# Optimization experiments

Measured on AMD Instinct MI355X. Metric: run time of the kernel, lower is better.

Reference implementation:

```python
import jax, jax.numpy as jnp
import numpy as np

TOP_K = 8
THRESHOLD = 0.0        # similarity_threshold
SELF_SIM = 0.999       # exclude_self cutoff
EPS = 1e-12            # F.normalize eps


def _l2_normalize(x):
    # matches torch.nn.functional.normalize(p=2, dim=-1, eps=1e-12)
    n = jnp.linalg.norm(x, axis=-1, keepdims=True)
    return x / jnp.maximum(n, EPS)


def setup_inputs() -> dict:
    key = jax.random.key(0)
    kq, km = jax.random.split(key)
    B, N, D = 2048, 65536, 512
    q = jax.random.normal(kq, (B, D), dtype=jnp.float32)
    mem = jax.random.normal(km, (N, D), dtype=jnp.float32)
    # add_memories() stores L2-normalized representations when normalize=True
    mem = _l2_normalize(mem)
    return {"query_representations": q, "memory_bank": mem}


def reference(query_representations, memory_bank):
    # normalize queries (config.normalize_memories=True)
    q = _l2_normalize(query_representations)            # [B, D]
    # cosine similarity: bank rows already unit-norm
    sims = jnp.einsum("bd,nd->bn", q, memory_bank)      # [B, N]
    neg_inf = jnp.float32(-jnp.inf)
    # exclude_self: mask near-exact matches
    sims = jnp.where(sims > SELF_SIM, neg_inf, sims)
    # threshold mask
    sims = jnp.where(sims >= THRESHOLD, sims, neg_inf)
    # top-k (k = min(top_k, count) = TOP_K since bank is full)
    top_sims, top_idx = jax.lax.top_k(sims, TOP_K)      # [B, K]
    retrieved = memory_bank[top_idx]                    # [B, K, D] gather
    mask = top_sims > neg_inf                           # [B, K] valid entries
    return retrieved, top_sims, mask
```

## Files before the change

kernel.cpp:

```cpp
#include <hip/hip_runtime.h>
#include <math.h>

#define D        512
#define NQ       2048
#define NMEM     65536
#define TOPK     8
#define NCAND    32
#define SELF_SIM 0.999f
#define FSCALE   64.0f
#define TAU_RAW  483.328f
#define CAP      448
#define SCAP     768

#define QB     128
#define SPAN   1024
#define NROUND 32
#define BUFSZ  16384u

typedef __attribute__((ext_vector_type(4))) float f32x4;
typedef __attribute__((ext_vector_type(4))) int   i32x4;
typedef __attribute__((ext_vector_type(8))) int   i32x8;

__device__ __forceinline__ void gl_lds16(const void* g, void* l) {
    __builtin_amdgcn_global_load_lds(
        (const __attribute__((address_space(1))) void*)g,
        (__attribute__((address_space(3))) void*)l, 16, 0, 0);
}

__device__ __forceinline__ unsigned pack4_fp8(float4 v) {
    int lo = __builtin_amdgcn_cvt_pk_fp8_f32(v.x * FSCALE, v.y * FSCALE, 0, false);
    return (unsigned)__builtin_amdgcn_cvt_pk_fp8_f32(v.z * FSCALE, v.w * FSCALE, lo, true);
}

__global__ __launch_bounds__(256)
void k_prep(const float* __restrict__ mem, const float* __restrict__ q,
            unsigned* __restrict__ mp8, unsigned* __restrict__ qp8,
            double* __restrict__ qinv)
{
    if (blockIdx.x < 2048) {
        const int i = blockIdx.x * 256 + threadIdx.x;
        const int row = i >> 3, p = i & 7;
        const float4* pf = (const float4*)(mem + (size_t)row * D + p * 64);
        float4 f[16];
        #pragma unroll
        for (int t = 0; t < 16; ++t) f[t] = pf[t];
        const int nblk = row >> 7, t8 = (row >> 4) & 7, fc = row & 15;
        const int kq = p >> 1, fb = (p & 1) * 2;
        uint4* dst = (uint4*)mp8 + ((size_t)nblk * 4096 + kq * 1024 + t8 * 128);
        #pragma unroll
        for (int u = 0; u < 2; ++u)
            #pragma unroll
            for (int h = 0; h < 2; ++h) {
                uint4 c;
                c.x = pack4_fp8(f[u * 8 + h * 4 + 0]);
                c.y = pack4_fp8(f[u * 8 + h * 4 + 1]);
                c.z = pack4_fp8(f[u * 8 + h * 4 + 2]);
                c.w = pack4_fp8(f[u * 8 + h * 4 + 3]);
                dst[h * 64 + (fb + u) * 16 + fc] = c;
            }
    } else {
        __shared__ float rb[4][512];
        const int wv = threadIdx.x >> 6, lane = threadIdx.x & 63;
        const int row = (blockIdx.x - 2048) * 4 + wv;
        const float4* src = (const float4*)(q + (size_t)row * D);
        float4 v0 = src[lane];
        float4 v1 = src[lane + 64];
        double ss = (double)v0.x*v0.x + (double)v0.y*v0.y + (double)v0.z*v0.z + (double)v0.w*v0.w
                  + (double)v1.x*v1.x + (double)v1.y*v1.y + (double)v1.z*v1.z + (double)v1.w*v1.w;
        #pragma unroll
        for (int off = 32; off >= 1; off >>= 1)
            ss += __shfl_xor(ss, off, 64);
        double inv = 1.0 / fmax(sqrt(ss), 1e-12);
        float invf = (float)inv;
        ((float4*)rb[wv])[lane]      = make_float4(v0.x*invf, v0.y*invf, v0.z*invf, v0.w*invf);
        ((float4*)rb[wv])[lane + 64] = make_float4(v1.x*invf, v1.y*invf, v1.z*invf, v1.w*invf);
        if (lane == 0) qinv[row] = inv;
        __syncthreads();
        if (lane < 32) {
            const int kq = lane >> 3, fr = (lane >> 1) & 3, h = lane & 1;
            const float* f = rb[wv] + kq * 128 + fr * 32 + h * 16;
            uint4 c;
            c.x = pack4_fp8(*(const float4*)(f));
            c.y = pack4_fp8(*(const float4*)(f + 4));
            c.z = pack4_fp8(*(const float4*)(f + 8));
            c.w = pack4_fp8(*(const float4*)(f + 12));
            const int qblk = row >> 6, t4 = (row >> 4) & 3, fc = row & 15;
            ((uint4*)qp8)[(size_t)qblk * 2048 + kq * 512 + t4 * 128 + h * 64 + fr * 16 + fc] = c;
        }
    }
}

__global__ __launch_bounds__(256, 4)
void k_cand(const char* __restrict__ qp8, const char* __restrict__ mp8,
            unsigned* __restrict__ cnt, uint2* __restrict__ cbuf)
{
    __shared__ __align__(16) char smem[32768 + 16 + SCAP * 8];
    unsigned* scnt = (unsigned*)(smem + 32768);
    uint2*    sbuf = (uint2*)   (smem + 32784);

    const int tid = threadIdx.x;
    const int w = tid >> 6, l = tid & 63;
    const int fc = l & 15, fr = l >> 4;

    const int id  = blockIdx.x;
    const int xcd = id & 7;
    const int j   = id >> 3;
    const int qblk = j & 15;
    const int sg   = j >> 4;
    const int split = xcd + 8 * sg;
    const int qbase = qblk * QB;
    const int nbase = split * SPAN;

    const char* qpan = qp8 + (size_t)(qblk * 2 + (w >> 1)) * 32768u
                           + (unsigned)(w & 1) * 4096u + (unsigned)l * 16u;
    const unsigned mpanel = (unsigned)(nbase >> 7) * 65536u;

    if (tid == 0) *scnt = 0u;

    f32x4 acc[2][8];
    const int lofs = l * 16;

#define STAGE(R, B)                                                            \
    {   const unsigned r_ = (unsigned)(R);                                     \
        const unsigned base_ = mpanel + (r_ >> 2) * 65536u + (r_ & 3u) * 16384u; \
        gl_lds16(mp8 + base_ + (unsigned)tid * 16u,          smem + (B) + (unsigned)tid * 16u); \
        gl_lds16(mp8 + base_ + (unsigned)tid * 16u + 4096u,  smem + (B) + (unsigned)tid * 16u + 4096u); \
        gl_lds16(mp8 + base_ + (unsigned)tid * 16u + 8192u,  smem + (B) + (unsigned)tid * 16u + 8192u); \
        gl_lds16(mp8 + base_ + (unsigned)tid * 16u + 12288u, smem + (B) + (unsigned)tid * 16u + 12288u); \
    }

    unsigned cb = 0u;
    STAGE(0, cb);

    for (int r = 0; r < NROUND; ++r) {
        const int kq = r & 3, sub = r >> 2;
        if (kq == 0) {
            #pragma unroll
            for (int jj = 0; jj < 2; ++jj)
                #pragma unroll
                for (int t = 0; t < 8; ++t) acc[jj][t] = (f32x4){0.f, 0.f, 0.f, 0.f};
        }
        asm volatile("" ::: "memory");
        __builtin_amdgcn_s_barrier();
        asm volatile("" ::: "memory");
        i32x4 qa0, qa1, qb0, qb1;
        {
            const char* qa = qpan + (unsigned)kq * 8192u;
            asm volatile("global_load_dwordx4 %0, %1, off"             : "=v"(qa0) : "v"(qa) : "memory");
            asm volatile("global_load_dwordx4 %0, %1, off offset:1024" : "=v"(qa1) : "v"(qa) : "memory");
            asm volatile("global_load_dwordx4 %0, %1, off offset:2048" : "=v"(qb0) : "v"(qa) : "memory");
            asm volatile("global_load_dwordx4 %0, %1, off offset:3072" : "=v"(qb1) : "v"(qa) : "memory");
        }
        if (r + 1 < NROUND) {
            STAGE(r + 1, cb ^ BUFSZ);
            asm volatile("s_waitcnt vmcnt(4)" ::: "memory");
        } else {
            asm volatile("s_waitcnt vmcnt(0)" ::: "memory");
        }
        __builtin_amdgcn_sched_barrier(0);
        __builtin_amdgcn_s_barrier();
        asm volatile("" ::: "memory");

        {
            const char* Ms = smem + cb;
            const i32x8 bv0 = __builtin_shufflevector(qa0, qa1, 0, 1, 2, 3, 4, 5, 6, 7);
            const i32x8 bv1 = __builtin_shufflevector(qb0, qb1, 0, 1, 2, 3, 4, 5, 6, 7);
            __builtin_amdgcn_s_setprio(1);
            #pragma unroll
            for (int t = 0; t < 8; ++t) {
                i32x4 lo = *(const i32x4*)(Ms + t * 2048 + lofs);
                i32x4 hi = *(const i32x4*)(Ms + t * 2048 + 1024 + lofs);
                i32x8 av = __builtin_shufflevector(lo, hi, 0, 1, 2, 3, 4, 5, 6, 7);
                acc[0][t] = __builtin_amdgcn_mfma_scale_f32_16x16x128_f8f6f4(
                              av, bv0, acc[0][t], 0, 0, 0, 0x7F7F7F7F, 0, 0x7F7F7F7F);
                acc[1][t] = __builtin_amdgcn_mfma_scale_f32_16x16x128_f8f6f4(
                              av, bv1, acc[1][t], 0, 0, 0, 0x7F7F7F7F, 0, 0x7F7F7F7F);
            }
            __builtin_amdgcn_s_setprio(0);
        }
        if (kq == 3) {
            const int nb0 = nbase + sub * 128 + fr * 4;
            #pragma unroll
            for (int jj = 0; jj < 2; ++jj) {
                const unsigned qloc = (unsigned)(w * 32 + jj * 16 + fc);
                #pragma unroll
                for (int t = 0; t < 8; ++t) {
                    const float tm = fmaxf(fmaxf(acc[jj][t][0], acc[jj][t][1]),
                                           fmaxf(acc[jj][t][2], acc[jj][t][3]));
                    if (tm > TAU_RAW) {
                        #pragma unroll
                        for (int rr = 0; rr < 4; ++rr) {
                            const float v = acc[jj][t][rr];
                            if (v > TAU_RAW) {
                                unsigned p = atomicAdd(scnt, 1u);
                                if (p < SCAP)
                                    sbuf[p] = make_uint2(__float_as_uint(v),
                                        (qloc << 16) | (unsigned)(nb0 + t * 16 + rr));
                            }
                        }
                    }
                }
            }
        }
        cb ^= BUFSZ;
    }
#undef STAGE

    __syncthreads();
    const unsigned ns = min(*scnt, (unsigned)SCAP);
    for (unsigned i = tid; i < ns; i += 256) {
        const uint2 e = sbuf[i];
        const int qg = qbase + (int)(e.y >> 16);
        const unsigned p = atomicAdd(&cnt[qg], 1u);
        if (p < CAP)
            cbuf[(size_t)qg * CAP + p] = make_uint2(e.x, e.y & 0xffffu);
    }
}

__global__ __launch_bounds__(256)
void k_final(const unsigned* __restrict__ cnt, const uint2* __restrict__ cbuf,
             const float* __restrict__ q, const float* __restrict__ mem,
             const double* __restrict__ qinv, float* __restrict__ out)
{
    __shared__ unsigned long long keys[CAP];
    __shared__ int    scand[NCAND];
    __shared__ double rsv[NCAND];
    __shared__ int    fidx[TOPK];

    const int qq  = blockIdx.x;
    const int tid = threadIdx.x;
    const int n = (int)min(cnt[qq], (unsigned)CAP);

    if (tid < NCAND) scand[tid] = -1;
    const uint2* src = cbuf + (size_t)qq * CAP;
    for (int c = tid; c < n; c += 256) {
        const uint2 e = src[c];
        keys[c] = ((unsigned long long)e.x << 16)
                | (unsigned long long)(0xffffu - (e.y & 0xffffu));
    }
    __syncthreads();
    for (int c = tid; c < n; c += 256) {
        const unsigned long long my = keys[c];
        int rank = 0;
        for (int j2 = 0; j2 < n; ++j2) rank += (keys[j2] > my) ? 1 : 0;
        if (rank < NCAND) scand[rank] = 0xffff - (int)(my & 0xffffu);
    }
    __syncthreads();

    const int w = tid >> 6, lane = tid & 63;
    float qv[8];
    #pragma unroll
    for (int t = 0; t < 8; ++t) qv[t] = q[(size_t)qq * D + t * 64 + lane];
    for (int ci = w * 8; ci < w * 8 + 8; ++ci) {
        const int m = scand[ci];
        double s = 0.0;
        if (m >= 0) {
            const float* mp = mem + (size_t)m * D;
            #pragma unroll
            for (int t = 0; t < 8; ++t)
                s += (double)qv[t] * (double)mp[t * 64 + lane];
        }
        #pragma unroll
        for (int off = 32; off >= 1; off >>= 1)
            s += __shfl_xor(s, off, 64);
        if (lane == 0) rsv[ci] = (m >= 0) ? s * qinv[qq] : -1.0 / 0.0;
    }
    __syncthreads();

    if (tid < NCAND) {
        double x = rsv[tid];
        if (scand[tid] < 0 || x > (double)SELF_SIM || x < 0.0) x = -1.0 / 0.0;
        rsv[tid] = x;
    }
    __syncthreads();
    if (tid < NCAND) {
        const double x  = rsv[tid];
        const int    mi = (scand[tid] < 0) ? 0x7fffffff : scand[tid];
        int rank = 0;
        for (int j2 = 0; j2 < NCAND; ++j2) {
            const double xj = rsv[j2];
            const int    ij = (scand[j2] < 0) ? 0x7fffffff : scand[j2];
            if (xj > x || (xj == x && (ij < mi || (ij == mi && j2 < tid)))) ++rank;
        }
        if (rank < TOPK) {
            float* tops  = out + (size_t)NQ * TOPK * D;
            float* maskp = tops + (size_t)NQ * TOPK;
            tops [qq * TOPK + rank] = (float)x;
            maskp[qq * TOPK + rank] = (x == -INFINITY) ? 0.0f : 1.0f;
            fidx [rank] = (scand[tid] < 0) ? 0 : scand[tid];
        }
    }
    __syncthreads();

    for (int i = tid; i < TOPK * (D / 4); i += 256) {
        const int s2 = i >> 7;
        const int d4 = i & 127;
        const int sr = fidx[s2];
        ((float4*)out)[((size_t)qq * TOPK + s2) * (D / 4) + d4] =
            ((const float4*)mem)[(size_t)sr * (D / 4) + d4];
    }
}

extern "C" void kernel_launch(void* const* d_in, const int* in_sizes, int n_in,
                              void* d_out, int out_size, void* d_ws, size_t ws_size,
                              hipStream_t stream)
{
    const float* q   = (const float*)d_in[0];
    const float* mem = (const float*)d_in[1];
    float* out = (float*)d_out;
    char* ws = (char*)d_ws;

    unsigned* mp8  = (unsigned*)(ws);
    unsigned* qp8  = (unsigned*)(ws + ((size_t)32 << 20));
    unsigned* cnt  = (unsigned*)(ws + ((size_t)33 << 20));
    uint2*    cbuf = (uint2*)   (ws + ((size_t)34 << 20));
    double*   qinv = (double*)  (ws + ((size_t)42 << 20));

    hipMemsetAsync(cnt, 0, NQ * sizeof(unsigned), stream);

    k_prep<<<2560, 256, 0, stream>>>(mem, q, mp8, qp8, qinv);
    k_cand<<<(NQ / QB) * (NMEM / SPAN), 256, 0, stream>>>((const char*)qp8, (const char*)mp8, cnt, cbuf);
    k_final<<<NQ, 256, 0, stream>>>(cnt, cbuf, q, mem, qinv, out);
}
```

Baseline: 185.0 us.

## Stage query tiles in LDS and split candidate kernel across 8 waves

The candidate kernel now runs 512 threads per block. Query fp8 panels are staged into LDS alongside memory panels through global_load_lds, replacing the per-wave direct global loads. The 8 waves split the block's 128 queries and 128 memory rows into 4x2 groups, so each wave holds half the accumulators. The per-query counter memset is folded into the prep kernel, which removes one launch. The trade-off is double the LDS footprint, which can lower occupancy, and larger barrier groups.

```diff
diff --git a/kernel.cpp b/kernel.cpp
--- a/kernel.cpp
+++ b/kernel.cpp
@@ -15,7 +15,7 @@
 #define QB     128
 #define SPAN   1024
 #define NROUND 32
-#define BUFSZ  16384u
+#define BUFSZ  32768u
 
 typedef __attribute__((ext_vector_type(4))) float f32x4;
 typedef __attribute__((ext_vector_type(4))) int   i32x4;
@@ -32,12 +32,21 @@
     return (unsigned)__builtin_amdgcn_cvt_pk_fp8_f32(v.z * FSCALE, v.w * FSCALE, lo, true);
 }
 
+__device__ __forceinline__ i32x8 ldpair(const char* p) {
+    const i32x4 a = *(const i32x4*)p;
+    const i32x4 b = *(const i32x4*)(p + 1024);
+    return __builtin_shufflevector(a, b, 0, 1, 2, 3, 4, 5, 6, 7);
+}
+
 __global__ __launch_bounds__(256)
 void k_prep(const float* __restrict__ mem, const float* __restrict__ q,
             unsigned* __restrict__ mp8, unsigned* __restrict__ qp8,
-            double* __restrict__ qinv)
+            double* __restrict__ qinv, unsigned* __restrict__ cnt)
 {
     if (blockIdx.x < 2048) {
+        if (blockIdx.x == 0) {
+            for (int c = threadIdx.x; c < NQ; c += 256) cnt[c] = 0u;
+        }
         const int i = blockIdx.x * 256 + threadIdx.x;
         const int row = i >> 3, p = i & 7;
         const float4* pf = (const float4*)(mem + (size_t)row * D + p * 64);
@@ -90,17 +99,18 @@
     }
 }
 
-__global__ __launch_bounds__(256, 4)
+__global__ __launch_bounds__(512, 4)
 void k_cand(const char* __restrict__ qp8, const char* __restrict__ mp8,
             unsigned* __restrict__ cnt, uint2* __restrict__ cbuf)
 {
-    __shared__ __align__(16) char smem[32768 + 16 + SCAP * 8];
-    unsigned* scnt = (unsigned*)(smem + 32768);
-    uint2*    sbuf = (uint2*)   (smem + 32784);
+    __shared__ __align__(16) char smem[65536 + 16 + SCAP * 8];
+    unsigned* scnt = (unsigned*)(smem + 65536);
+    uint2*    sbuf = (uint2*)   (smem + 65552);
 
     const int tid = threadIdx.x;
     const int w = tid >> 6, l = tid & 63;
     const int fc = l & 15, fr = l >> 4;
+    const int qg = w & 3, ng = w >> 2;
 
     const int id  = blockIdx.x;
     const int xcd = id & 7;
@@ -111,26 +121,27 @@
     const int qbase = qblk * QB;
     const int nbase = split * SPAN;
 
-    const char* qpan = qp8 + (size_t)(qblk * 2 + (w >> 1)) * 32768u
-                           + (unsigned)(w & 1) * 4096u + (unsigned)l * 16u;
-    const unsigned mpanel = (unsigned)(nbase >> 7) * 65536u;
+    const char* qs0 = qp8 + (size_t)(qblk * 2 + 0) * 32768u + (unsigned)tid * 16u;
+    const char* qs1 = qp8 + (size_t)(qblk * 2 + 1) * 32768u + (unsigned)tid * 16u;
+    const char* ms  = mp8 + (size_t)(nbase >> 7) * 65536u + (unsigned)tid * 16u;
 
     if (tid == 0) *scnt = 0u;
 
-    f32x4 acc[2][8];
+    f32x4 acc[2][4];
     const int lofs = l * 16;
 
 #define STAGE(R, B)                                                            \
     {   const unsigned r_ = (unsigned)(R);                                     \
-        const unsigned base_ = mpanel + (r_ >> 2) * 65536u + (r_ & 3u) * 16384u; \
-        gl_lds16(mp8 + base_ + (unsigned)tid * 16u,          smem + (B) + (unsigned)tid * 16u); \
-        gl_lds16(mp8 + base_ + (unsigned)tid * 16u + 4096u,  smem + (B) + (unsigned)tid * 16u + 4096u); \
-        gl_lds16(mp8 + base_ + (unsigned)tid * 16u + 8192u,  smem + (B) + (unsigned)tid * 16u + 8192u); \
-        gl_lds16(mp8 + base_ + (unsigned)tid * 16u + 12288u, smem + (B) + (unsigned)tid * 16u + 12288u); \
-    }
-
+        const unsigned kq_ = (r_ & 3u);                                        \
+        const unsigned mo_ = (r_ >> 2) * 65536u + kq_ * 16384u;                \
+        gl_lds16(qs0 + kq_ * 8192u, smem + (B) + (unsigned)tid * 16u);         \
+        gl_lds16(qs1 + kq_ * 8192u, smem + (B) + 8192u + (unsigned)tid * 16u); \
+        gl_lds16(ms + mo_,          smem + (B) + 16384u + (unsigned)tid * 16u);\
+        gl_lds16(ms + mo_ + 8192u,  smem + (B) + 24576u + (unsigned)tid * 16u);\
+    }
+
+    STAGE(0, 0u);
     unsigned cb = 0u;
-    STAGE(0, cb);
 
     for (int r = 0; r < NROUND; ++r) {
         const int kq = r & 3, sub = r >> 2;
@@ -138,19 +149,11 @@
             #pragma unroll
             for (int jj = 0; jj < 2; ++jj)
                 #pragma unroll
-                for (int t = 0; t < 8; ++t) acc[jj][t] = (f32x4){0.f, 0.f, 0.f, 0.f};
+                for (int t = 0; t < 4; ++t) acc[jj][t] = (f32x4){0.f, 0.f, 0.f, 0.f};
         }
         asm volatile("" ::: "memory");
         __builtin_amdgcn_s_barrier();
         asm volatile("" ::: "memory");
-        i32x4 qa0, qa1, qb0, qb1;
-        {
-            const char* qa = qpan + (unsigned)kq * 8192u;
-            asm volatile("global_load_dwordx4 %0, %1, off"             : "=v"(qa0) : "v"(qa) : "memory");
-            asm volatile("global_load_dwordx4 %0, %1, off offset:1024" : "=v"(qa1) : "v"(qa) : "memory");
-            asm volatile("global_load_dwordx4 %0, %1, off offset:2048" : "=v"(qb0) : "v"(qa) : "memory");
-            asm volatile("global_load_dwordx4 %0, %1, off offset:3072" : "=v"(qb1) : "v"(qa) : "memory");
-        }
         if (r + 1 < NROUND) {
             STAGE(r + 1, cb ^ BUFSZ);
             asm volatile("s_waitcnt vmcnt(4)" ::: "memory");
@@ -162,15 +165,14 @@
         asm volatile("" ::: "memory");
 
         {
-            const char* Ms = smem + cb;
-            const i32x8 bv0 = __builtin_shufflevector(qa0, qa1, 0, 1, 2, 3, 4, 5, 6, 7);
-            const i32x8 bv1 = __builtin_shufflevector(qb0, qb1, 0, 1, 2, 3, 4, 5, 6, 7);
+            const char* Qb = smem + cb + (unsigned)qg * 4096u;
+            const char* Mb = smem + cb + 16384u + (unsigned)ng * 8192u;
+            const i32x8 bv0 = ldpair(Qb + lofs);
+            const i32x8 bv1 = ldpair(Qb + 2048 + lofs);
             __builtin_amdgcn_s_setprio(1);
             #pragma unroll
-            for (int t = 0; t < 8; ++t) {
-                i32x4 lo = *(const i32x4*)(Ms + t * 2048 + lofs);
-                i32x4 hi = *(const i32x4*)(Ms + t * 2048 + 1024 + lofs);
-                i32x8 av = __builtin_shufflevector(lo, hi, 0, 1, 2, 3, 4, 5, 6, 7);
+            for (int t = 0; t < 4; ++t) {
+                const i32x8 av = ldpair(Mb + t * 2048 + lofs);
                 acc[0][t] = __builtin_amdgcn_mfma_scale_f32_16x16x128_f8f6f4(
                               av, bv0, acc[0][t], 0, 0, 0, 0x7F7F7F7F, 0, 0x7F7F7F7F);
                 acc[1][t] = __builtin_amdgcn_mfma_scale_f32_16x16x128_f8f6f4(
@@ -179,12 +181,12 @@
             __builtin_amdgcn_s_setprio(0);
         }
         if (kq == 3) {
-            const int nb0 = nbase + sub * 128 + fr * 4;
             #pragma unroll
             for (int jj = 0; jj < 2; ++jj) {
-                const unsigned qloc = (unsigned)(w * 32 + jj * 16 + fc);
+                const unsigned qloc = (unsigned)(qg * 32 + jj * 16 + fc);
                 #pragma unroll
-                for (int t = 0; t < 8; ++t) {
+                for (int t = 0; t < 4; ++t) {
+                    const int nb0 = nbase + sub * 128 + (ng * 4 + t) * 16 + fr * 4;
                     const float tm = fmaxf(fmaxf(acc[jj][t][0], acc[jj][t][1]),
                                            fmaxf(acc[jj][t][2], acc[jj][t][3]));
                     if (tm > TAU_RAW) {
@@ -195,7 +197,7 @@
                                 unsigned p = atomicAdd(scnt, 1u);
                                 if (p < SCAP)
                                     sbuf[p] = make_uint2(__float_as_uint(v),
-                                        (qloc << 16) | (unsigned)(nb0 + t * 16 + rr));
+                                        (qloc << 16) | (unsigned)(nb0 + rr));
                             }
                         }
                     }
@@ -208,12 +210,12 @@
 
     __syncthreads();
     const unsigned ns = min(*scnt, (unsigned)SCAP);
-    for (unsigned i = tid; i < ns; i += 256) {
+    for (unsigned i = tid; i < ns; i += 512) {
         const uint2 e = sbuf[i];
-        const int qg = qbase + (int)(e.y >> 16);
-        const unsigned p = atomicAdd(&cnt[qg], 1u);
+        const int qg2 = qbase + (int)(e.y >> 16);
+        const unsigned p = atomicAdd(&cnt[qg2], 1u);
         if (p < CAP)
-            cbuf[(size_t)qg * CAP + p] = make_uint2(e.x, e.y & 0xffffu);
+            cbuf[(size_t)qg2 * CAP + p] = make_uint2(e.x, e.y & 0xffffu);
     }
 }
 
@@ -316,9 +318,7 @@
     uint2*    cbuf = (uint2*)   (ws + ((size_t)34 << 20));
     double*   qinv = (double*)  (ws + ((size_t)42 << 20));
 
-    hipMemsetAsync(cnt, 0, NQ * sizeof(unsigned), stream);
-
-    k_prep<<<2560, 256, 0, stream>>>(mem, q, mp8, qp8, qinv);
-    k_cand<<<(NQ / QB) * (NMEM / SPAN), 256, 0, stream>>>((const char*)qp8, (const char*)mp8, cnt, cbuf);
+    k_prep<<<2560, 256, 0, stream>>>(mem, q, mp8, qp8, qinv, cnt);
+    k_cand<<<(NQ / QB) * (NMEM / SPAN), 512, 0, stream>>>((const char*)qp8, (const char*)mp8, cnt, cbuf);
     k_final<<<NQ, 256, 0, stream>>>(cnt, cbuf, q, mem, qinv, out);
 }
```

After: 198.5 us. 1.07x slower.
